# Optimization experiments

Hardware: AMD Instinct MI355X
Metric: run time of the kernel (lower is better)

The kernel has to match this reference:

```python
import jax, jax.numpy as jnp
import numpy as np

B, S, D_IN, D_OUT = 4, 2048, 1024, 1024


def setup_inputs() -> dict:
    key = jax.random.key(0)
    k1, k2, k3, k4 = jax.random.split(key, 4)
    scale = 1.0 / np.sqrt(D_IN)
    return {
        "x": jax.random.normal(k1, (B, S, D_IN), dtype=jnp.float32),
        "W_q": jax.random.normal(k2, (D_OUT, D_IN), dtype=jnp.float32) * scale,
        "W_k": jax.random.normal(k3, (D_OUT, D_IN), dtype=jnp.float32) * scale,
        "W_v": jax.random.normal(k4, (D_OUT, D_IN), dtype=jnp.float32) * scale,
    }


def reference(x, W_q, W_k, W_v):
    # torch nn.Linear: y = x @ W.T (bias=False)
    q = jnp.einsum("bsd,od->bso", x, W_q)
    k = jnp.einsum("bsd,od->bso", x, W_k)
    v = jnp.einsum("bsd,od->bso", x, W_v)
    s = q.shape[1]
    scores = jnp.einsum("bqo,bko->bqk", q, k)  # [B, S, S]
    causal = jnp.triu(jnp.ones((s, s), dtype=bool), k=1)
    scores = jnp.where(causal, -jnp.inf, scores)
    inv_sqrt_d = 1.0 / jnp.sqrt(jnp.asarray(q.shape[-1], scores.dtype))
    attn = jax.nn.softmax(scores * inv_sqrt_d, axis=-1)
    # dropout p=0.0 -> identity (deterministic reference)
    return jnp.einsum("bqk,bko->bqo", attn, v)
```

## Files before the change

kernel.cpp:

```cpp
#include <hip/hip_runtime.h>

typedef unsigned short u16;
typedef unsigned int u32;
typedef __bf16 bf16x8 __attribute__((ext_vector_type(8)));
typedef float f32x4 __attribute__((ext_vector_type(4)));

#define AS1 __attribute__((address_space(1)))
#define AS3 __attribute__((address_space(3)))

__device__ inline u16 f2bf(float f) {
  union { float f; unsigned u; } a; a.f = f;
  unsigned u = a.u;
  return (u16)((u + 0x7fffu + ((u >> 16) & 1u)) >> 16);
}
__device__ inline float bf2f(u16 h) {
  union { unsigned u; float f; } a; a.u = ((u32)h) << 16; return a.f;
}

__global__ __launch_bounds__(256) void cvt_all_kernel(
    const float* __restrict__ x, const float* __restrict__ wq,
    const float* __restrict__ wk, const float* __restrict__ wv,
    u16* __restrict__ xb, u16* __restrict__ wqb,
    u16* __restrict__ wkb, u16* __restrict__ wvb) {
  int bid = blockIdx.x;
  const float* in; u16* out;
  if (bid < 8192) { in = x; out = xb; }
  else if (bid < 9216) { in = wq; out = wqb; bid -= 8192; }
  else if (bid < 10240) { in = wk; out = wkb; bid -= 9216; }
  else { in = wv; out = wvb; bid -= 10240; }
  size_t i = ((size_t)bid * 256 + threadIdx.x) * 4;
  float4 v = *(const float4*)(in + i);
  ushort4 o;
  o.x = f2bf(v.x); o.y = f2bf(v.y); o.z = f2bf(v.z); o.w = f2bf(v.w);
  *(ushort4*)(out + i) = o;
}

template <typename CT, int BN>
__device__ __forceinline__ void gemm_core(
    u16* __restrict__ lds,
    const u16* __restrict__ A, const u16* __restrict__ B, CT* __restrict__ C,
    int nt, int lda, int ldb, int ldc, int m0, int n0) {
  constexpr int ABUF = 16384;
  constexpr int BBUF = BN * 64;
  constexpr int BSW = BN / 64;
  constexpr int NI = BN / 64;

  const int tid = threadIdx.x;
  const int ln = tid & 63, wv = tid >> 6;
  const int wr = wv >> 2, wc = wv & 3;

  auto sweep = [&](const u16* src, int ld, int t, int s, int base) {
    const int c = s * 512 + tid;
    const int row = c >> 3, slot = c & 7;
    const int col = (slot ^ (row & 7)) * 8;
    __builtin_amdgcn_global_load_lds(
        (const AS1 void*)(src + (size_t)row * ld + (size_t)t * 64 + col),
        (AS3 void*)(&lds[base + c * 8]), 16, 0, 0);
  };

  f32x4 acc[8][NI] = {};

#pragma unroll
  for (int s = 0; s < BSW; ++s) sweep(B, ldb, 0, s, 2 * ABUF);
#pragma unroll
  for (int s = 0; s < 4; ++s) sweep(A, lda, 0, s, 0);
  if (nt > 1) {
#pragma unroll
    for (int s = 0; s < BSW; ++s) sweep(B, ldb, 1, s, 2 * ABUF + BBUF);
#pragma unroll
    for (int s = 0; s < 4; ++s) sweep(A, lda, 1, s, ABUF);
    if constexpr (BSW == 4) asm volatile("s_waitcnt vmcnt(8)" ::: "memory");
    else                    asm volatile("s_waitcnt vmcnt(6)" ::: "memory");
  } else {
    asm volatile("s_waitcnt vmcnt(0)" ::: "memory");
  }
  __builtin_amdgcn_s_barrier();

  for (int t = 0; t < nt; ++t) {
    const int p = t & 1;
    const u16* La = &lds[p * ABUF];
    const u16* Lb = &lds[2 * ABUF + p * BBUF];
    bf16x8 bfr[NI][2];
#pragma unroll
    for (int q = 0; q < 4; ++q) {
      if (q == 0) {
        __builtin_amdgcn_sched_barrier(0);
#pragma unroll
        for (int ni = 0; ni < NI; ++ni)
#pragma unroll
          for (int ks = 0; ks < 2; ++ks) {
            const int row = wc * (BN / 4) + ni * 16 + (ln & 15);
            const int kc = ks * 4 + (ln >> 4);
            bfr[ni][ks] = *(const bf16x8*)&Lb[row * 64 + ((kc ^ (row & 7)) << 3)];
          }
      }
      bf16x8 afr[2][2];
#pragma unroll
      for (int mi = 0; mi < 2; ++mi)
#pragma unroll
        for (int ks = 0; ks < 2; ++ks) {
          const int row = wr * 128 + (q * 2 + mi) * 16 + (ln & 15);
          const int kc = ks * 4 + (ln >> 4);
          afr[mi][ks] = *(const bf16x8*)&La[row * 64 + ((kc ^ (row & 7)) << 3)];
        }
      if (q == 0)      { if (t >= 1 && t + 1 < nt) { sweep(A, lda, t + 1, 0, (p ^ 1) * ABUF); sweep(A, lda, t + 1, 1, (p ^ 1) * ABUF); } }
      else if (q == 1) { if (t >= 1 && t + 1 < nt) { sweep(A, lda, t + 1, 2, (p ^ 1) * ABUF); sweep(A, lda, t + 1, 3, (p ^ 1) * ABUF); } }
      else if (q == 2) { if (t + 2 < nt) { sweep(B, ldb, t + 2, 0, 2 * ABUF + p * BBUF); if (BSW == 4) sweep(B, ldb, t + 2, 1, 2 * ABUF + p * BBUF); } }
      else             { if (t + 2 < nt) { if (BSW == 4) { sweep(B, ldb, t + 2, 2, 2 * ABUF + p * BBUF); sweep(B, ldb, t + 2, 3, 2 * ABUF + p * BBUF); } else { sweep(B, ldb, t + 2, 1, 2 * ABUF + p * BBUF); } } }

      __builtin_amdgcn_s_barrier();
      __builtin_amdgcn_s_setprio(1);
#pragma unroll
      for (int mi = 0; mi < 2; ++mi)
#pragma unroll
        for (int ni = 0; ni < NI; ++ni)
#pragma unroll
          for (int ks = 0; ks < 2; ++ks)
            acc[q * 2 + mi][ni] = __builtin_amdgcn_mfma_f32_16x16x32_bf16(
                afr[mi][ks], bfr[ni][ks], acc[q * 2 + mi][ni], 0, 0, 0);
      __builtin_amdgcn_s_setprio(0);
      if (q == 3) {
        if (t + 2 < nt) {
          if constexpr (BSW == 4) asm volatile("s_waitcnt vmcnt(4)" ::: "memory");
          else                    asm volatile("s_waitcnt vmcnt(2)" ::: "memory");
        } else if (t + 1 < nt) {
          asm volatile("s_waitcnt vmcnt(0)" ::: "memory");
        }
      }
      __builtin_amdgcn_s_barrier();
    }
  }

#pragma unroll
  for (int mi = 0; mi < 8; ++mi) {
    const int rbase = m0 + wr * 128 + mi * 16 + (ln >> 4) * 4;
#pragma unroll
    for (int ni = 0; ni < NI; ++ni) {
      const int col = n0 + wc * (BN / 4) + ni * 16 + (ln & 15);
#pragma unroll
      for (int r = 0; r < 4; ++r) {
        const float v = acc[mi][ni][r];
        CT* ptr = &C[(size_t)(rbase + r) * ldc + col];
        if constexpr (sizeof(CT) == 4) *(float*)ptr = v;
        else                           *ptr = f2bf(v);
      }
    }
  }
}

__global__ __launch_bounds__(512, 2) void proj_qk_kernel(
    const u16* __restrict__ xb, const u16* __restrict__ wqb,
    const u16* __restrict__ wkb, u16* __restrict__ Qb, u16* __restrict__ Kb) {
  __shared__ __align__(16) u16 lds[65536];
  const int bid = blockIdx.x;
  const int w = bid >> 7, r = bid & 127;
  const int rb = r >> 2, n0 = (r & 3) * 256;
  const u16* B = w ? wkb : wqb;
  u16* C = w ? Kb : Qb;
  gemm_core<u16, 256>(lds, xb + (size_t)rb * 256 * 1024, B + (size_t)n0 * 1024,
                      C, 16, 1024, 1024, 1024, rb * 256, n0);
}

__global__ __launch_bounds__(512, 2) void qktvt_kernel(
    const u16* __restrict__ Qb, const u16* __restrict__ Kb, u16* __restrict__ Sb16,
    const u16* __restrict__ wvb, const u16* __restrict__ xb, u16* __restrict__ VTb) {
  __shared__ __align__(16) u16 lds[65536];
  const int bid = blockIdx.x;
  const int item = (bid & 7) * 32 + (bid >> 3);
  if (item < 144) {
    const int z = item / 36, xt = item % 36;
    int m = 0;
    while ((m + 1) * (m + 2) / 2 <= xt) ++m;
    const int n = xt - m * (m + 1) / 2;
    gemm_core<u16, 256>(lds,
        Qb + ((size_t)z * 2048 + m * 256) * 1024,
        Kb + ((size_t)z * 2048 + n * 256) * 1024,
        Sb16 + (size_t)z * 2048 * 2048,
        16, 1024, 1024, 2048, m * 256, n * 256);
  } else {
    const int j = item - 144;
    const int z = j / 28, r2 = j % 28, d = r2 / 7, kb = r2 % 7;
    gemm_core<u16, 256>(lds, wvb + (size_t)d * 256 * 1024,
                        xb + (size_t)z * 2048 * 1024 + (size_t)kb * 256 * 1024,
                        VTb + (size_t)z * 1024 * 2048,
                        16, 1024, 1024, 2048, d * 256, kb * 256);
  }
}

__global__ __launch_bounds__(512, 2) void smvt_kernel(
    u16* __restrict__ Sb16, float* __restrict__ R,
    const u16* __restrict__ wvb, const u16* __restrict__ xb) {
  __shared__ __align__(16) u16 lds[65536];
  const int bid = blockIdx.x;
  const int tid = threadIdx.x;
  if (bid < 64) {
    const int z = bid >> 4, r = bid & 15;
    const int d = r >> 2, h = r & 3;
    const u16* A = wvb + (size_t)d * 256 * 1024 + h * 256;
    const u16* B = xb + ((size_t)z * 2048 + 1792) * 1024 + h * 256;
    float* C = R + (size_t)z * 2097152 + (d * 4 + h) * 65536;
    gemm_core<float, 256>(lds, A, B, C, 4, 1024, 1024, 256, 0, 0);
    return;
  }
  const int j = bid - 64;
  const int m = 7 - (j >> 6), z = (j >> 4) & 3, s = j & 15;
  const int iters = (m + 2) >> 1;
  const int wvid = tid >> 6, lane = tid & 63;
  u16* S0 = Sb16 + (size_t)z * 2048 * 2048;
  for (int rr = wvid; rr < 16; rr += 8) {
    const int r = m * 256 + s * 16 + rr;
    u16* row = S0 + (size_t)r * 2048;
    float vals[4][8];
    float mx = -3.4e38f;
#pragma unroll
    for (int it2 = 0; it2 < 4; ++it2)
      if (it2 < iters) {
        const int idx8 = it2 * 512 + lane * 8;
        uint4 w = *(const uint4*)(row + idx8);
        const u32 ws[4] = {w.x, w.y, w.z, w.w};
#pragma unroll
        for (int e = 0; e < 8; ++e) {
          const u16 hb = (u16)(ws[e >> 1] >> ((e & 1) * 16));
          const float xv = bf2f(hb) * 0.03125f;
          vals[it2][e] = (idx8 + e <= r) ? xv : -3.4e38f;
          mx = fmaxf(mx, vals[it2][e]);
        }
      }
#pragma unroll
    for (int o = 32; o; o >>= 1) mx = fmaxf(mx, __shfl_xor(mx, o, 64));
    float sum = 0.f;
#pragma unroll
    for (int it2 = 0; it2 < 4; ++it2)
      if (it2 < iters) {
#pragma unroll
        for (int e = 0; e < 8; ++e) {
          const float pp = __expf(vals[it2][e] - mx);
          vals[it2][e] = pp;
          sum += pp;
        }
      }
#pragma unroll
    for (int o = 32; o; o >>= 1) sum += __shfl_xor(sum, o, 64);
    const float rcp = 1.f / sum;
#pragma unroll
    for (int it2 = 0; it2 < 4; ++it2)
      if (it2 < iters) {
        const int idx8 = it2 * 512 + lane * 8;
        uint4 w;
        u32 wo[4];
#pragma unroll
        for (int e2 = 0; e2 < 4; ++e2) {
          const u16 lo = f2bf(vals[it2][e2 * 2] * rcp);
          const u16 hi = f2bf(vals[it2][e2 * 2 + 1] * rcp);
          wo[e2] = (u32)lo | ((u32)hi << 16);
        }
        w.x = wo[0]; w.y = wo[1]; w.z = wo[2]; w.w = wo[3];
        *(uint4*)(row + idx8) = w;
      }
  }
}

__global__ __launch_bounds__(256) void vtfix_kernel(const float* __restrict__ R,
                                                    u16* __restrict__ VTb) {
  const int bid = blockIdx.x;
  const int z = bid >> 3, q = bid & 7;
  const int d = q >> 1, rh = q & 1;
  const float* P0 = R + (size_t)z * 2097152 + (d * 4 + 0) * 65536;
  const float* P1 = P0 + 65536;
  const float* P2 = P0 + 131072;
  const float* P3 = P0 + 196608;
  for (int k = threadIdx.x; k < 128 * 64; k += 256) {
    const int dp = rh * 128 + (k >> 6), c4 = (k & 63) * 4;
    const size_t off = (size_t)dp * 256 + c4;
    float4 a = *(const float4*)(P0 + off);
    float4 b = *(const float4*)(P1 + off);
    float4 c = *(const float4*)(P2 + off);
    float4 e = *(const float4*)(P3 + off);
    ushort4 o;
    o.x = f2bf(a.x + b.x + c.x + e.x); o.y = f2bf(a.y + b.y + c.y + e.y);
    o.z = f2bf(a.z + b.z + c.z + e.z); o.w = f2bf(a.w + b.w + c.w + e.w);
    *(ushort4*)(VTb + (size_t)z * 1024 * 2048 + (size_t)(d * 256 + dp) * 2048 +
                1792 + c4) = o;
  }
}

__constant__ signed char CPM[16] = {5,5,7,7,7,6,4,4,6,6,3,3,1,2,2,0};
__constant__ signed char CPK[16] = {0,12,0,11,22,0,0,10,10,19,0,8,0,0,6,0};
__constant__ signed char CPN[16] = {12,12,11,11,10,10,10,10,9,9,8,8,8,6,6,4};
__constant__ signed char CPS[16] = {0,1,0,1,2,0,0,1,1,2,0,1,0,0,1,0};

__global__ __launch_bounds__(512, 2) void pv_kernel(
    const u16* __restrict__ P, const u16* __restrict__ VTb,
    float* __restrict__ out, char* __restrict__ R) {
  __shared__ __align__(16) u16 lds[65536];
  const int cls = blockIdx.x, n = blockIdx.y;
  const size_t z = blockIdx.z;
  const int m = CPM[cls], k0 = CPK[cls], ntc = CPN[cls], sl = CPS[cls];
  const u16* Ap = P + z * 2048 * 2048 + (size_t)m * 256 * 2048 + (size_t)k0 * 64;
  const u16* Bp = VTb + z * 1024 * 2048 + (size_t)n * 256 * 2048 + (size_t)k0 * 64;
  if (sl == 0) {
    gemm_core<float, 256>(lds, Ap, Bp, out + z * 2048 * 1024, ntc,
                          2048, 2048, 1024, m * 256, n * 256);
  } else if (sl == 1) {
    u16* s1 = (u16*)(R + z * (8ul << 20) + (4ul << 20)) - (size_t)512 * 1024;
    gemm_core<u16, 256>(lds, Ap, Bp, s1, ntc, 2048, 2048, 1024, m * 256, n * 256);
  } else {
    u16* s2 = (u16*)(R + z * (8ul << 20) + (7ul << 20)) - (size_t)1536 * 1024;
    gemm_core<u16, 256>(lds, Ap, Bp, s2, ntc, 2048, 2048, 1024, m * 256, n * 256);
  }
}

__global__ __launch_bounds__(256) void reduce_kernel(float* __restrict__ out,
                                                     const char* __restrict__ R) {
  const int j = blockIdx.x;
  const int m = 2 + (j >> 5), z = (j >> 3) & 3, s = j & 7;
  float* ob = out + (size_t)z * 2048 * 1024;
  const u16* s1 = (const u16*)(R + (size_t)z * (8ul << 20) + (4ul << 20));
  const u16* s2 = (const u16*)(R + (size_t)z * (8ul << 20) + (7ul << 20));
  const int r0 = m * 256 + s * 32;
  for (int k = threadIdx.x; k < 32 * 256; k += 256) {
    const int rr = r0 + (k >> 8), cc = k & 255;
    float4 o = ((float4*)(ob + (size_t)rr * 1024))[cc];
    ushort4 a = ((const ushort4*)(s1 + (size_t)(rr - 512) * 1024))[cc];
    o.x += bf2f(a.x); o.y += bf2f(a.y); o.z += bf2f(a.z); o.w += bf2f(a.w);
    if (m >= 6) {
      ushort4 b = ((const ushort4*)(s2 + (size_t)(rr - 1536) * 1024))[cc];
      o.x += bf2f(b.x); o.y += bf2f(b.y); o.z += bf2f(b.z); o.w += bf2f(b.w);
    }
    ((float4*)(ob + (size_t)rr * 1024))[cc] = o;
  }
}

extern "C" void kernel_launch(void* const* d_in, const int* in_sizes, int n_in,
                              void* d_out, int out_size, void* d_ws, size_t ws_size,
                              hipStream_t stream) {
  const float* x  = (const float*)d_in[0];
  const float* Wq = (const float*)d_in[1];
  const float* Wk = (const float*)d_in[2];
  const float* Wv = (const float*)d_in[3];
  float* out = (float*)d_out;

  char* ws = (char*)d_ws;
  u16* xb   = (u16*)(ws);
  u16* wqb  = (u16*)(ws + (16ul << 20));
  u16* wkb  = (u16*)(ws + (18ul << 20));
  u16* wvb  = (u16*)(ws + (20ul << 20));
  u16* Qb   = (u16*)(ws + (22ul << 20));
  u16* Kb   = (u16*)(ws + (38ul << 20));
  u16* VTb  = (u16*)(ws + (54ul << 20));
  u16* Sb16 = (u16*)(ws + (70ul << 20));
  char* R   = ws + (102ul << 20);

  cvt_all_kernel<<<11264, 256, 0, stream>>>(x, Wq, Wk, Wv, xb, wqb, wkb, wvb);

  proj_qk_kernel<<<256, 512, 0, stream>>>(xb, wqb, wkb, Qb, Kb);

  qktvt_kernel<<<256, 512, 0, stream>>>(Qb, Kb, Sb16, wvb, xb, VTb);

  smvt_kernel<<<576, 512, 0, stream>>>(Sb16, (float*)R, wvb, xb);

  vtfix_kernel<<<32, 256, 0, stream>>>((const float*)R, VTb);

  pv_kernel<<<dim3(16, 4, 4), 512, 0, stream>>>(Sb16, VTb, out, R);

  reduce_kernel<<<192, 256, 0, stream>>>(out, R);
}
```

Baseline: 161.0 us.

## Triple-buffer A tiles in GEMM core to prefetch two k-steps ahead

Replaces the double-buffered A tile with a three-slot ring in LDS so A loads for step t+2 are issued during step t, alongside B. The per-block LDS allocation grows to 160KB. The aim is to hide global-to-LDS latency with a deeper prefetch. The larger LDS footprint likely allows only one block per CU instead of two, reducing occupancy.

After: 162.6 us. No clear change (+1.0%).

```diff
diff --git a/kernel.cpp b/kernel.cpp
--- a/kernel.cpp
+++ b/kernel.cpp
@@ -35,16 +35,11 @@
   *(ushort4*)(out + i) = o;
 }
 
-template <typename CT, int BN>
-__device__ __forceinline__ void gemm_core(
+template <typename CT>
+__device__ __forceinline__ void gemm_core3(
     u16* __restrict__ lds,
     const u16* __restrict__ A, const u16* __restrict__ B, CT* __restrict__ C,
     int nt, int lda, int ldb, int ldc, int m0, int n0) {
-  constexpr int ABUF = 16384;
-  constexpr int BBUF = BN * 64;
-  constexpr int BSW = BN / 64;
-  constexpr int NI = BN / 64;
-
   const int tid = threadIdx.x;
   const int ln = tid & 63, wv = tid >> 6;
   const int wr = wv >> 2, wc = wv & 3;
@@ -58,38 +53,38 @@
         (AS3 void*)(&lds[base + c * 8]), 16, 0, 0);
   };
 
-  f32x4 acc[8][NI] = {};
-
-#pragma unroll
-  for (int s = 0; s < BSW; ++s) sweep(B, ldb, 0, s, 2 * ABUF);
+  f32x4 acc[8][4] = {};
+
+#pragma unroll
+  for (int s = 0; s < 4; ++s) sweep(B, ldb, 0, s, 49152);
 #pragma unroll
   for (int s = 0; s < 4; ++s) sweep(A, lda, 0, s, 0);
   if (nt > 1) {
 #pragma unroll
-    for (int s = 0; s < BSW; ++s) sweep(B, ldb, 1, s, 2 * ABUF + BBUF);
-#pragma unroll
-    for (int s = 0; s < 4; ++s) sweep(A, lda, 1, s, ABUF);
-    if constexpr (BSW == 4) asm volatile("s_waitcnt vmcnt(8)" ::: "memory");
-    else                    asm volatile("s_waitcnt vmcnt(6)" ::: "memory");
+    for (int s = 0; s < 4; ++s) sweep(B, ldb, 1, s, 65536);
+#pragma unroll
+    for (int s = 0; s < 4; ++s) sweep(A, lda, 1, s, 16384);
+    asm volatile("s_waitcnt vmcnt(8)" ::: "memory");
   } else {
     asm volatile("s_waitcnt vmcnt(0)" ::: "memory");
   }
   __builtin_amdgcn_s_barrier();
 
   for (int t = 0; t < nt; ++t) {
-    const int p = t & 1;
-    const u16* La = &lds[p * ABUF];
-    const u16* Lb = &lds[2 * ABUF + p * BBUF];
-    bf16x8 bfr[NI][2];
+    const u16* La = &lds[(t % 3) * 16384];
+    const u16* Lb = &lds[49152 + (t & 1) * 16384];
+    const int an = ((t + 2) % 3) * 16384;
+    const int bn = 49152 + (t & 1) * 16384;
+    bf16x8 bfr[4][2];
 #pragma unroll
     for (int q = 0; q < 4; ++q) {
       if (q == 0) {
         __builtin_amdgcn_sched_barrier(0);
 #pragma unroll
-        for (int ni = 0; ni < NI; ++ni)
+        for (int ni = 0; ni < 4; ++ni)
 #pragma unroll
           for (int ks = 0; ks < 2; ++ks) {
-            const int row = wc * (BN / 4) + ni * 16 + (ln & 15);
+            const int row = wc * 64 + ni * 16 + (ln & 15);
             const int kc = ks * 4 + (ln >> 4);
             bfr[ni][ks] = *(const bf16x8*)&Lb[row * 64 + ((kc ^ (row & 7)) << 3)];
           }
@@ -103,29 +98,27 @@
           const int kc = ks * 4 + (ln >> 4);
           afr[mi][ks] = *(const bf16x8*)&La[row * 64 + ((kc ^ (row & 7)) << 3)];
         }
-      if (q == 0)      { if (t >= 1 && t + 1 < nt) { sweep(A, lda, t + 1, 0, (p ^ 1) * ABUF); sweep(A, lda, t + 1, 1, (p ^ 1) * ABUF); } }
-      else if (q == 1) { if (t >= 1 && t + 1 < nt) { sweep(A, lda, t + 1, 2, (p ^ 1) * ABUF); sweep(A, lda, t + 1, 3, (p ^ 1) * ABUF); } }
-      else if (q == 2) { if (t + 2 < nt) { sweep(B, ldb, t + 2, 0, 2 * ABUF + p * BBUF); if (BSW == 4) sweep(B, ldb, t + 2, 1, 2 * ABUF + p * BBUF); } }
-      else             { if (t + 2 < nt) { if (BSW == 4) { sweep(B, ldb, t + 2, 2, 2 * ABUF + p * BBUF); sweep(B, ldb, t + 2, 3, 2 * ABUF + p * BBUF); } else { sweep(B, ldb, t + 2, 1, 2 * ABUF + p * BBUF); } } }
+      if (t + 2 < nt) {
+        if (q == 0)      { sweep(A, lda, t + 2, 0, an); sweep(A, lda, t + 2, 1, an); }
+        else if (q == 1) { sweep(A, lda, t + 2, 2, an); sweep(A, lda, t + 2, 3, an); }
+        else if (q == 2) { sweep(B, ldb, t + 2, 0, bn); sweep(B, ldb, t + 2, 1, bn); }
+        else             { sweep(B, ldb, t + 2, 2, bn); sweep(B, ldb, t + 2, 3, bn); }
+      }
 
       __builtin_amdgcn_s_barrier();
       __builtin_amdgcn_s_setprio(1);
 #pragma unroll
       for (int mi = 0; mi < 2; ++mi)
 #pragma unroll
-        for (int ni = 0; ni < NI; ++ni)
+        for (int ni = 0; ni < 4; ++ni)
 #pragma unroll
           for (int ks = 0; ks < 2; ++ks)
             acc[q * 2 + mi][ni] = __builtin_amdgcn_mfma_f32_16x16x32_bf16(
                 afr[mi][ks], bfr[ni][ks], acc[q * 2 + mi][ni], 0, 0, 0);
       __builtin_amdgcn_s_setprio(0);
       if (q == 3) {
-        if (t + 2 < nt) {
-          if constexpr (BSW == 4) asm volatile("s_waitcnt vmcnt(4)" ::: "memory");
-          else                    asm volatile("s_waitcnt vmcnt(2)" ::: "memory");
-        } else if (t + 1 < nt) {
-          asm volatile("s_waitcnt vmcnt(0)" ::: "memory");
-        }
+        if (t + 2 < nt)      asm volatile("s_waitcnt vmcnt(8)" ::: "memory");
+        else if (t + 1 < nt) asm volatile("s_waitcnt vmcnt(0)" ::: "memory");
       }
       __builtin_amdgcn_s_barrier();
     }
@@ -135,8 +128,8 @@
   for (int mi = 0; mi < 8; ++mi) {
     const int rbase = m0 + wr * 128 + mi * 16 + (ln >> 4) * 4;
 #pragma unroll
-    for (int ni = 0; ni < NI; ++ni) {
-      const int col = n0 + wc * (BN / 4) + ni * 16 + (ln & 15);
+    for (int ni = 0; ni < 4; ++ni) {
+      const int col = n0 + wc * 64 + ni * 16 + (ln & 15);
 #pragma unroll
       for (int r = 0; r < 4; ++r) {
         const float v = acc[mi][ni][r];
@@ -151,20 +144,20 @@
 __global__ __launch_bounds__(512, 2) void proj_qk_kernel(
     const u16* __restrict__ xb, const u16* __restrict__ wqb,
     const u16* __restrict__ wkb, u16* __restrict__ Qb, u16* __restrict__ Kb) {
-  __shared__ __align__(16) u16 lds[65536];
+  __shared__ __align__(16) u16 lds[81920];
   const int bid = blockIdx.x;
   const int w = bid >> 7, r = bid & 127;
   const int rb = r >> 2, n0 = (r & 3) * 256;
   const u16* B = w ? wkb : wqb;
   u16* C = w ? Kb : Qb;
-  gemm_core<u16, 256>(lds, xb + (size_t)rb * 256 * 1024, B + (size_t)n0 * 1024,
-                      C, 16, 1024, 1024, 1024, rb * 256, n0);
+  gemm_core3<u16>(lds, xb + (size_t)rb * 256 * 1024, B + (size_t)n0 * 1024,
+                  C, 16, 1024, 1024, 1024, rb * 256, n0);
 }
 
 __global__ __launch_bounds__(512, 2) void qktvt_kernel(
     const u16* __restrict__ Qb, const u16* __restrict__ Kb, u16* __restrict__ Sb16,
     const u16* __restrict__ wvb, const u16* __restrict__ xb, u16* __restrict__ VTb) {
-  __shared__ __align__(16) u16 lds[65536];
+  __shared__ __align__(16) u16 lds[81920];
   const int bid = blockIdx.x;
   const int item = (bid & 7) * 32 + (bid >> 3);
   if (item < 144) {
@@ -172,7 +165,7 @@
     int m = 0;
     while ((m + 1) * (m + 2) / 2 <= xt) ++m;
     const int n = xt - m * (m + 1) / 2;
-    gemm_core<u16, 256>(lds,
+    gemm_core3<u16>(lds,
         Qb + ((size_t)z * 2048 + m * 256) * 1024,
         Kb + ((size_t)z * 2048 + n * 256) * 1024,
         Sb16 + (size_t)z * 2048 * 2048,
@@ -180,17 +173,17 @@
   } else {
     const int j = item - 144;
     const int z = j / 28, r2 = j % 28, d = r2 / 7, kb = r2 % 7;
-    gemm_core<u16, 256>(lds, wvb + (size_t)d * 256 * 1024,
-                        xb + (size_t)z * 2048 * 1024 + (size_t)kb * 256 * 1024,
-                        VTb + (size_t)z * 1024 * 2048,
-                        16, 1024, 1024, 2048, d * 256, kb * 256);
+    gemm_core3<u16>(lds, wvb + (size_t)d * 256 * 1024,
+                    xb + (size_t)z * 2048 * 1024 + (size_t)kb * 256 * 1024,
+                    VTb + (size_t)z * 1024 * 2048,
+                    16, 1024, 1024, 2048, d * 256, kb * 256);
   }
 }
 
 __global__ __launch_bounds__(512, 2) void smvt_kernel(
     u16* __restrict__ Sb16, float* __restrict__ R,
     const u16* __restrict__ wvb, const u16* __restrict__ xb) {
-  __shared__ __align__(16) u16 lds[65536];
+  __shared__ __align__(16) u16 lds[81920];
   const int bid = blockIdx.x;
   const int tid = threadIdx.x;
   if (bid < 64) {
@@ -199,7 +192,7 @@
     const u16* A = wvb + (size_t)d * 256 * 1024 + h * 256;
     const u16* B = xb + ((size_t)z * 2048 + 1792) * 1024 + h * 256;
     float* C = R + (size_t)z * 2097152 + (d * 4 + h) * 65536;
-    gemm_core<float, 256>(lds, A, B, C, 4, 1024, 1024, 256, 0, 0);
+    gemm_core3<float>(lds, A, B, C, 4, 1024, 1024, 256, 0, 0);
     return;
   }
   const int j = bid - 64;
@@ -292,21 +285,21 @@
 __global__ __launch_bounds__(512, 2) void pv_kernel(
     const u16* __restrict__ P, const u16* __restrict__ VTb,
     float* __restrict__ out, char* __restrict__ R) {
-  __shared__ __align__(16) u16 lds[65536];
+  __shared__ __align__(16) u16 lds[81920];
   const int cls = blockIdx.x, n = blockIdx.y;
   const size_t z = blockIdx.z;
   const int m = CPM[cls], k0 = CPK[cls], ntc = CPN[cls], sl = CPS[cls];
   const u16* Ap = P + z * 2048 * 2048 + (size_t)m * 256 * 2048 + (size_t)k0 * 64;
   const u16* Bp = VTb + z * 1024 * 2048 + (size_t)n * 256 * 2048 + (size_t)k0 * 64;
   if (sl == 0) {
-    gemm_core<float, 256>(lds, Ap, Bp, out + z * 2048 * 1024, ntc,
-                          2048, 2048, 1024, m * 256, n * 256);
+    gemm_core3<float>(lds, Ap, Bp, out + z * 2048 * 1024, ntc,
+                      2048, 2048, 1024, m * 256, n * 256);
   } else if (sl == 1) {
     u16* s1 = (u16*)(R + z * (8ul << 20) + (4ul << 20)) - (size_t)512 * 1024;
-    gemm_core<u16, 256>(lds, Ap, Bp, s1, ntc, 2048, 2048, 1024, m * 256, n * 256);
+    gemm_core3<u16>(lds, Ap, Bp, s1, ntc, 2048, 2048, 1024, m * 256, n * 256);
   } else {
     u16* s2 = (u16*)(R + z * (8ul << 20) + (7ul << 20)) - (size_t)1536 * 1024;
-    gemm_core<u16, 256>(lds, Ap, Bp, s2, ntc, 2048, 2048, 1024, m * 256, n * 256);
+    gemm_core3<u16>(lds, Ap, Bp, s2, ntc, 2048, 2048, 1024, m * 256, n * 256);
   }
 }
 
```
